# Optimization experiments

Hardware: AMD Instinct MI355X
Metric: run time of the kernel (lower is better)

## Reference

```python
import jax, jax.numpy as jnp
import numpy as np

N_POINTS = 1048576
FEATURES = 64
RES = 256


def setup_inputs() -> dict:
    key = jax.random.key(0)
    k1, k2, k3, k4 = jax.random.split(key, 4)
    x = jax.random.uniform(k1, (N_POINTS, 3), jnp.float32, -1.0, 1.0)
    plane_xy = jax.random.normal(k2, (1, FEATURES, RES, RES), jnp.float32)
    plane_xz = jax.random.normal(k3, (1, FEATURES, RES, RES), jnp.float32)
    plane_yz = jax.random.normal(k4, (1, FEATURES, RES, RES), jnp.float32)
    pose = jnp.zeros((1,), jnp.float32)
    person_id = 0
    return {"x": x, "plane_xy": plane_xy, "plane_xz": plane_xz,
            "plane_yz": plane_yz, "pose": pose, "person_id": person_id}


def _grid_sample_points(plane, uv):
    """Bilinear sample. plane: [1,C,IH,IW], uv: [N,2] in [-1,1]. Returns [N,C].
    Matches the hand-rolled torch grid_sample (align_corners=True semantics,
    corner indices clamped, weights computed from unclamped floor coords)."""
    C, IH, IW = plane.shape[1], plane.shape[2], plane.shape[3]
    ix = (uv[:, 0] + 1.0) * 0.5 * (IW - 1)
    iy = (uv[:, 1] + 1.0) * 0.5 * (IH - 1)
    fx0 = jnp.floor(ix)
    fy0 = jnp.floor(iy)
    # bilinear weights (differentiable w.r.t. ix, iy)
    w_nw = (fx0 + 1.0 - ix) * (fy0 + 1.0 - iy)
    w_ne = (ix - fx0) * (fy0 + 1.0 - iy)
    w_sw = (fx0 + 1.0 - ix) * (iy - fy0)
    w_se = (ix - fx0) * (iy - fy0)
    # clamped integer corner indices (non-differentiable, as in torch no_grad)
    x0 = jnp.clip(fx0, 0, IW - 1).astype(jnp.int32)
    x1 = jnp.clip(fx0 + 1.0, 0, IW - 1).astype(jnp.int32)
    y0 = jnp.clip(fy0, 0, IH - 1).astype(jnp.int32)
    y1 = jnp.clip(fy0 + 1.0, 0, IH - 1).astype(jnp.int32)
    pf = plane.reshape(C, IH * IW)  # [C, IH*IW]
    v_nw = pf[:, y0 * IW + x0]  # [C, N]
    v_ne = pf[:, y0 * IW + x1]
    v_sw = pf[:, y1 * IW + x0]
    v_se = pf[:, y1 * IW + x1]
    out = v_nw * w_nw + v_ne * w_ne + v_sw * w_sw + v_se * w_se  # [C, N]
    return out.T  # [N, C]


def reference(x, plane_xy, plane_xz, plane_yz, pose, person_id):
    # person_id selects the (single) person's planes; pose is unused upstream.
    feat_xy = _grid_sample_points(plane_xy, x[:, [0, 1]])
    feat_xz = _grid_sample_points(plane_xz, x[:, [0, 2]])
    feat_yz = _grid_sample_points(plane_yz, x[:, [1, 2]])
    feat = (feat_xy + feat_xz + feat_yz) / 3.0  # [N, FEATURES]
    return feat
```

## Files before the change

### kernel.cpp

```cpp
#include <hip/hip_runtime.h>

#define N_POINTS 1048576
#define FEAT 64
#define RES 256
#define PLANE_ELEMS (FEAT * RES * RES)

#define BUCKET_G 32
#define NBUCKET (BUCKET_G * BUCKET_G * BUCKET_G)

#define SAMPLE_BLOCKS (N_POINTS / 32)
#define SAMPLE_CPX (SAMPLE_BLOCKS / 8)

typedef unsigned short ushort_t;
typedef float v4f __attribute__((ext_vector_type(4)));

__device__ __forceinline__ ushort_t f2bf(float f) {
  unsigned u = __float_as_uint(f);
  unsigned r = u + 0x7FFFu + ((u >> 16) & 1u);
  return (ushort_t)(r >> 16);
}

__global__ __launch_bounds__(256) void transpose_bf16(
    const float* __restrict__ pxy, const float* __restrict__ pxz,
    const float* __restrict__ pyz, ushort_t* __restrict__ dst) {
  __shared__ ushort_t tile[64][72];
  const int plane = blockIdx.y;
  const float* src = (plane == 0) ? pxy : ((plane == 1) ? pxz : pyz);
  ushort_t* out = dst + (size_t)plane * PLANE_ELEMS;
  const int p0 = blockIdx.x * 64;
  const int tid = threadIdx.x;
#pragma unroll
  for (int k = 0; k < 4; ++k) {
    int c = (tid >> 4) + k * 16;
    int pp = (tid & 15) * 4;
    float4 v = *(const float4*)(src + (size_t)c * (RES * RES) + p0 + pp);
    tile[pp + 0][c] = f2bf(v.x);
    tile[pp + 1][c] = f2bf(v.y);
    tile[pp + 2][c] = f2bf(v.z);
    tile[pp + 3][c] = f2bf(v.w);
  }
  __syncthreads();
#pragma unroll
  for (int k = 0; k < 2; ++k) {
    int idx = k * 256 + tid;
    int pp = idx >> 3;
    int c8 = (idx & 7) * 8;
    uint4 v = *(const uint4*)&tile[pp][c8];
    *(uint4*)(out + (size_t)(p0 + pp) * FEAT + c8) = v;
  }
}

__device__ __forceinline__ unsigned part1by2(unsigned v) {
  v &= 0x3FFu;
  v = (v | (v << 16)) & 0x030000FFu;
  v = (v | (v << 8)) & 0x0300F00Fu;
  v = (v | (v << 4)) & 0x030C30C3u;
  v = (v | (v << 2)) & 0x09249249u;
  return v;
}

__device__ __forceinline__ unsigned morton_bucket(float px, float py, float pz) {
  int bx = (int)((px + 1.0f) * (0.5f * BUCKET_G));
  int by = (int)((py + 1.0f) * (0.5f * BUCKET_G));
  int bz = (int)((pz + 1.0f) * (0.5f * BUCKET_G));
  bx = min(max(bx, 0), BUCKET_G - 1);
  by = min(max(by, 0), BUCKET_G - 1);
  bz = min(max(bz, 0), BUCKET_G - 1);
  return part1by2((unsigned)bx) | (part1by2((unsigned)by) << 1) |
         (part1by2((unsigned)bz) << 2);
}

__global__ __launch_bounds__(256) void zero_hist(unsigned* __restrict__ h) {
  h[blockIdx.x * 256 + threadIdx.x] = 0u;
}

__global__ __launch_bounds__(256) void bucket_count(
    const float* __restrict__ x, unsigned* __restrict__ hist) {
  int n = blockIdx.x * 256 + threadIdx.x;
  float px = x[n * 3 + 0];
  float py = x[n * 3 + 1];
  float pz = x[n * 3 + 2];
  atomicAdd(&hist[morton_bucket(px, py, pz)], 1u);
}

__global__ __launch_bounds__(1024) void scan_hist(
    const unsigned* __restrict__ hist, unsigned* __restrict__ cursor) {
  __shared__ unsigned part[1024];
  const int tid = threadIdx.x;
  unsigned local[32];
  unsigned s = 0;
#pragma unroll
  for (int i = 0; i < 32; ++i) {
    local[i] = s;
    s += hist[tid * 32 + i];
  }
  part[tid] = s;
  __syncthreads();
  for (int off = 1; off < 1024; off <<= 1) {
    unsigned add = (tid >= off) ? part[tid - off] : 0u;
    __syncthreads();
    part[tid] += add;
    __syncthreads();
  }
  unsigned base = (tid == 0) ? 0u : part[tid - 1];
#pragma unroll
  for (int i = 0; i < 32; ++i) cursor[tid * 32 + i] = base + local[i];
}

__global__ __launch_bounds__(256) void bucket_scatter(
    const float* __restrict__ x, unsigned* __restrict__ cursor,
    float4* __restrict__ xs) {
  int n = blockIdx.x * 256 + threadIdx.x;
  float px = x[n * 3 + 0];
  float py = x[n * 3 + 1];
  float pz = x[n * 3 + 2];
  unsigned b = morton_bucket(px, py, pz);
  unsigned pos = atomicAdd(&cursor[b], 1u);
  xs[pos] = make_float4(px, py, pz, __uint_as_float((unsigned)n));
}

__device__ __forceinline__ void unpack_fma(uint4 v, float w, float* acc) {
  acc[0] = fmaf(__uint_as_float(v.x << 16), w, acc[0]);
  acc[1] = fmaf(__uint_as_float(v.x & 0xFFFF0000u), w, acc[1]);
  acc[2] = fmaf(__uint_as_float(v.y << 16), w, acc[2]);
  acc[3] = fmaf(__uint_as_float(v.y & 0xFFFF0000u), w, acc[3]);
  acc[4] = fmaf(__uint_as_float(v.z << 16), w, acc[4]);
  acc[5] = fmaf(__uint_as_float(v.z & 0xFFFF0000u), w, acc[5]);
  acc[6] = fmaf(__uint_as_float(v.w << 16), w, acc[6]);
  acc[7] = fmaf(__uint_as_float(v.w & 0xFFFF0000u), w, acc[7]);
}

__device__ __forceinline__ void sample_plane(const ushort_t* __restrict__ tp,
                                             float u, float v, int c8,
                                             float* acc) {
  float ix = (u + 1.0f) * 0.5f * (float)(RES - 1);
  float iy = (v + 1.0f) * 0.5f * (float)(RES - 1);
  float fx0 = floorf(ix), fy0 = floorf(iy);
  float wx1 = ix - fx0, wy1 = iy - fy0;
  float wx0 = fx0 + 1.0f - ix, wy0 = fy0 + 1.0f - iy;
  int x0 = min(max((int)fx0, 0), RES - 1);
  int y0 = min(max((int)fy0, 0), RES - 1);
  int x1 = min(max((int)fx0 + 1, 0), RES - 1);
  int y1 = min(max((int)fy0 + 1, 0), RES - 1);

  const uint4 v00 = *(const uint4*)(tp + (size_t)(y0 * RES + x0) * FEAT + c8);
  const uint4 v01 = *(const uint4*)(tp + (size_t)(y0 * RES + x1) * FEAT + c8);
  const uint4 v10 = *(const uint4*)(tp + (size_t)(y1 * RES + x0) * FEAT + c8);
  const uint4 v11 = *(const uint4*)(tp + (size_t)(y1 * RES + x1) * FEAT + c8);

  unpack_fma(v00, wx0 * wy0, acc);
  unpack_fma(v01, wx1 * wy0, acc);
  unpack_fma(v10, wx0 * wy1, acc);
  unpack_fma(v11, wx1 * wy1, acc);
}

__global__ __launch_bounds__(256) void triplane_sample_sorted(
    const float4* __restrict__ xs, const ushort_t* __restrict__ tps,
    float* __restrict__ out) {
  int bid = blockIdx.x;
  int swz = (bid & 7) * SAMPLE_CPX + (bid >> 3);
  int p = swz * 32 + (threadIdx.x >> 3);
  int c8 = (threadIdx.x & 7) << 3;

  v4f pt = __builtin_nontemporal_load((const v4f*)xs + p);
  unsigned n = __float_as_uint(pt.w);

  float acc[8] = {0.f, 0.f, 0.f, 0.f, 0.f, 0.f, 0.f, 0.f};
  sample_plane(tps, pt.x, pt.y, c8, acc);
  sample_plane(tps + PLANE_ELEMS, pt.x, pt.z, c8, acc);
  sample_plane(tps + 2 * PLANE_ELEMS, pt.y, pt.z, c8, acc);

  const float s = 1.0f / 3.0f;
  v4f lo = {acc[0] * s, acc[1] * s, acc[2] * s, acc[3] * s};
  v4f hi = {acc[4] * s, acc[5] * s, acc[6] * s, acc[7] * s};
  float* o = out + (size_t)n * FEAT + c8;
  __builtin_nontemporal_store(lo, (v4f*)o);
  __builtin_nontemporal_store(hi, (v4f*)(o + 4));
}

__global__ __launch_bounds__(256) void triplane_sample_bf16(
    const float* __restrict__ x, const ushort_t* __restrict__ tps,
    float* __restrict__ out) {
  int t = blockIdx.x * 256 + threadIdx.x;
  int n = t >> 3;
  int c8 = (t & 7) << 3;
  float px = __builtin_nontemporal_load(x + n * 3 + 0);
  float py = __builtin_nontemporal_load(x + n * 3 + 1);
  float pz = __builtin_nontemporal_load(x + n * 3 + 2);
  float acc[8] = {0.f, 0.f, 0.f, 0.f, 0.f, 0.f, 0.f, 0.f};
  sample_plane(tps, px, py, c8, acc);
  sample_plane(tps + PLANE_ELEMS, px, pz, c8, acc);
  sample_plane(tps + 2 * PLANE_ELEMS, py, pz, c8, acc);
  const float s = 1.0f / 3.0f;
  v4f lo = {acc[0] * s, acc[1] * s, acc[2] * s, acc[3] * s};
  v4f hi = {acc[4] * s, acc[5] * s, acc[6] * s, acc[7] * s};
  float* o = out + (size_t)n * FEAT + c8;
  __builtin_nontemporal_store(lo, (v4f*)o);
  __builtin_nontemporal_store(hi, (v4f*)(o + 4));
}

__device__ __forceinline__ float sample_one(const float* __restrict__ pc,
                                            float u, float v) {
  float ix = (u + 1.0f) * 0.5f * (float)(RES - 1);
  float iy = (v + 1.0f) * 0.5f * (float)(RES - 1);
  float fx0 = floorf(ix), fy0 = floorf(iy);
  float wx1 = ix - fx0, wy1 = iy - fy0;
  float wx0 = fx0 + 1.0f - ix, wy0 = fy0 + 1.0f - iy;
  int x0 = min(max((int)fx0, 0), RES - 1);
  int y0 = min(max((int)fy0, 0), RES - 1);
  int x1 = min(max((int)fx0 + 1, 0), RES - 1);
  int y1 = min(max((int)fy0 + 1, 0), RES - 1);
  return pc[y0 * RES + x0] * (wx0 * wy0) + pc[y0 * RES + x1] * (wx1 * wy0) +
         pc[y1 * RES + x0] * (wx0 * wy1) + pc[y1 * RES + x1] * (wx1 * wy1);
}

__global__ __launch_bounds__(256) void triplane_direct(
    const float* __restrict__ x, const float* __restrict__ pxy,
    const float* __restrict__ pxz, const float* __restrict__ pyz,
    float* __restrict__ out) {
  int t = blockIdx.x * 256 + threadIdx.x;
  int n = t >> 6;
  int c = t & 63;
  float px = x[n * 3 + 0];
  float py = x[n * 3 + 1];
  float pz = x[n * 3 + 2];
  const size_t cs = (size_t)c * (RES * RES);
  float acc = sample_one(pxy + cs, px, py) + sample_one(pxz + cs, px, pz) +
              sample_one(pyz + cs, py, pz);
  out[(size_t)n * FEAT + c] = acc * (1.0f / 3.0f);
}

extern "C" void kernel_launch(void* const* d_in, const int* in_sizes, int n_in,
                              void* d_out, int out_size, void* d_ws,
                              size_t ws_size, hipStream_t stream) {
  const float* x   = (const float*)d_in[0];
  const float* pxy = (const float*)d_in[1];
  const float* pxz = (const float*)d_in[2];
  const float* pyz = (const float*)d_in[3];
  float* out = (float*)d_out;

  const size_t tps_bytes = (size_t)3 * PLANE_ELEMS * sizeof(ushort_t);
  const size_t xs_bytes  = (size_t)N_POINTS * sizeof(float4);
  const size_t cnt_bytes = (size_t)NBUCKET * sizeof(unsigned);
  const size_t need_sorted = tps_bytes + xs_bytes + 2 * cnt_bytes;

  if (ws_size >= need_sorted) {
    ushort_t* tps    = (ushort_t*)d_ws;
    float4* xs       = (float4*)((char*)d_ws + tps_bytes);
    unsigned* cursor = (unsigned*)((char*)d_ws + tps_bytes + xs_bytes);
    unsigned* hist   = cursor + NBUCKET;

    dim3 tgrid(RES * RES / 64, 3);
    transpose_bf16<<<tgrid, 256, 0, stream>>>(pxy, pxz, pyz, tps);
    zero_hist<<<NBUCKET / 256, 256, 0, stream>>>(hist);
    bucket_count<<<N_POINTS / 256, 256, 0, stream>>>(x, hist);
    scan_hist<<<1, 1024, 0, stream>>>(hist, cursor);
    bucket_scatter<<<N_POINTS / 256, 256, 0, stream>>>(x, cursor, xs);
    triplane_sample_sorted<<<SAMPLE_BLOCKS, 256, 0, stream>>>(xs, tps, out);
  } else if (ws_size >= tps_bytes) {
    ushort_t* tps = (ushort_t*)d_ws;
    dim3 tgrid(RES * RES / 64, 3);
    transpose_bf16<<<tgrid, 256, 0, stream>>>(pxy, pxz, pyz, tps);
    triplane_sample_bf16<<<(N_POINTS * 8) / 256, 256, 0, stream>>>(x, tps, out);
  } else {
    triplane_direct<<<(N_POINTS * 64) / 256, 256, 0, stream>>>(x, pxy, pxz,
                                                               pyz, out);
  }
}
```

Before: 481.3 us.

## Fuse plane transpose with bucket count and store plane cache as fp16

```diff
diff --git a/kernel.cpp b/kernel.cpp
--- a/kernel.cpp
+++ b/kernel.cpp
@@ -11,43 +11,17 @@
 #define SAMPLE_BLOCKS (N_POINTS / 32)
 #define SAMPLE_CPX (SAMPLE_BLOCKS / 8)
 
+#define TRANSPOSE_BLOCKS (3 * (RES * RES / 64))
+#define COUNT_BLOCKS (N_POINTS / 256)
+#define PREP_BLOCKS (TRANSPOSE_BLOCKS + COUNT_BLOCKS)
+
 typedef unsigned short ushort_t;
 typedef float v4f __attribute__((ext_vector_type(4)));
-
-__device__ __forceinline__ ushort_t f2bf(float f) {
-  unsigned u = __float_as_uint(f);
-  unsigned r = u + 0x7FFFu + ((u >> 16) & 1u);
-  return (ushort_t)(r >> 16);
-}
-
-__global__ __launch_bounds__(256) void transpose_bf16(
-    const float* __restrict__ pxy, const float* __restrict__ pxz,
-    const float* __restrict__ pyz, ushort_t* __restrict__ dst) {
-  __shared__ ushort_t tile[64][72];
-  const int plane = blockIdx.y;
-  const float* src = (plane == 0) ? pxy : ((plane == 1) ? pxz : pyz);
-  ushort_t* out = dst + (size_t)plane * PLANE_ELEMS;
-  const int p0 = blockIdx.x * 64;
-  const int tid = threadIdx.x;
-#pragma unroll
-  for (int k = 0; k < 4; ++k) {
-    int c = (tid >> 4) + k * 16;
-    int pp = (tid & 15) * 4;
-    float4 v = *(const float4*)(src + (size_t)c * (RES * RES) + p0 + pp);
-    tile[pp + 0][c] = f2bf(v.x);
-    tile[pp + 1][c] = f2bf(v.y);
-    tile[pp + 2][c] = f2bf(v.z);
-    tile[pp + 3][c] = f2bf(v.w);
-  }
-  __syncthreads();
-#pragma unroll
-  for (int k = 0; k < 2; ++k) {
-    int idx = k * 256 + tid;
-    int pp = idx >> 3;
-    int c8 = (idx & 7) * 8;
-    uint4 v = *(const uint4*)&tile[pp][c8];
-    *(uint4*)(out + (size_t)(p0 + pp) * FEAT + c8) = v;
-  }
+typedef _Float16 half8 __attribute__((ext_vector_type(8)));
+
+__device__ __forceinline__ ushort_t f2h(float f) {
+  _Float16 h = (_Float16)f;
+  return __builtin_bit_cast(unsigned short, h);
 }
 
 __device__ __forceinline__ unsigned part1by2(unsigned v) {
@@ -70,17 +44,45 @@
          (part1by2((unsigned)bz) << 2);
 }
 
-__global__ __launch_bounds__(256) void zero_hist(unsigned* __restrict__ h) {
-  h[blockIdx.x * 256 + threadIdx.x] = 0u;
-}
-
-__global__ __launch_bounds__(256) void bucket_count(
+__global__ __launch_bounds__(256) void prep_transpose_count(
+    const float* __restrict__ pxy, const float* __restrict__ pxz,
+    const float* __restrict__ pyz, ushort_t* __restrict__ dst,
     const float* __restrict__ x, unsigned* __restrict__ hist) {
-  int n = blockIdx.x * 256 + threadIdx.x;
-  float px = x[n * 3 + 0];
-  float py = x[n * 3 + 1];
-  float pz = x[n * 3 + 2];
-  atomicAdd(&hist[morton_bucket(px, py, pz)], 1u);
+  const int b = blockIdx.x;
+  const int tid = threadIdx.x;
+  if (b >= TRANSPOSE_BLOCKS) {
+    int n = (b - TRANSPOSE_BLOCKS) * 256 + tid;
+    float px = x[n * 3 + 0];
+    float py = x[n * 3 + 1];
+    float pz = x[n * 3 + 2];
+    atomicAdd(&hist[morton_bucket(px, py, pz)], 1u);
+    return;
+  }
+  __shared__ ushort_t tile[64][72];
+  const int plane = b >> 10;
+  const int p0 = (b & 1023) * 64;
+  const float* src = (plane == 0) ? pxy : ((plane == 1) ? pxz : pyz);
+  ushort_t* out = dst + (size_t)plane * PLANE_ELEMS;
+#pragma unroll
+  for (int k = 0; k < 4; ++k) {
+    int c = (tid >> 4) + k * 16;
+    int pp = (tid & 15) * 4;
+    v4f v = __builtin_nontemporal_load(
+        (const v4f*)(src + (size_t)c * (RES * RES) + p0 + pp));
+    tile[pp + 0][c] = f2h(v.x);
+    tile[pp + 1][c] = f2h(v.y);
+    tile[pp + 2][c] = f2h(v.z);
+    tile[pp + 3][c] = f2h(v.w);
+  }
+  __syncthreads();
+#pragma unroll
+  for (int k = 0; k < 2; ++k) {
+    int idx = k * 256 + tid;
+    int pp = idx >> 3;
+    int c8 = (idx & 7) * 8;
+    uint4 v = *(const uint4*)&tile[pp][c8];
+    *(uint4*)(out + (size_t)(p0 + pp) * FEAT + c8) = v;
+  }
 }
 
 __global__ __launch_bounds__(1024) void scan_hist(
@@ -119,22 +121,16 @@
   xs[pos] = make_float4(px, py, pz, __uint_as_float((unsigned)n));
 }
 
-__device__ __forceinline__ void unpack_fma(uint4 v, float w, float* acc) {
-  acc[0] = fmaf(__uint_as_float(v.x << 16), w, acc[0]);
-  acc[1] = fmaf(__uint_as_float(v.x & 0xFFFF0000u), w, acc[1]);
-  acc[2] = fmaf(__uint_as_float(v.y << 16), w, acc[2]);
-  acc[3] = fmaf(__uint_as_float(v.y & 0xFFFF0000u), w, acc[3]);
-  acc[4] = fmaf(__uint_as_float(v.z << 16), w, acc[4]);
-  acc[5] = fmaf(__uint_as_float(v.z & 0xFFFF0000u), w, acc[5]);
-  acc[6] = fmaf(__uint_as_float(v.w << 16), w, acc[6]);
-  acc[7] = fmaf(__uint_as_float(v.w & 0xFFFF0000u), w, acc[7]);
+__device__ __forceinline__ void fma_mix8(half8 v, float w, float* acc) {
+#pragma unroll
+  for (int j = 0; j < 8; ++j) acc[j] = fmaf((float)v[j], w, acc[j]);
 }
 
 __device__ __forceinline__ void sample_plane(const ushort_t* __restrict__ tp,
                                              float u, float v, int c8,
                                              float* acc) {
-  float ix = (u + 1.0f) * 0.5f * (float)(RES - 1);
-  float iy = (v + 1.0f) * 0.5f * (float)(RES - 1);
+  float ix = fmaf(u, 0.5f * (float)(RES - 1), 0.5f * (float)(RES - 1));
+  float iy = fmaf(v, 0.5f * (float)(RES - 1), 0.5f * (float)(RES - 1));
   float fx0 = floorf(ix), fy0 = floorf(iy);
   float wx1 = ix - fx0, wy1 = iy - fy0;
   float wx0 = fx0 + 1.0f - ix, wy0 = fy0 + 1.0f - iy;
@@ -143,15 +139,15 @@
   int x1 = min(max((int)fx0 + 1, 0), RES - 1);
   int y1 = min(max((int)fy0 + 1, 0), RES - 1);
 
-  const uint4 v00 = *(const uint4*)(tp + (size_t)(y0 * RES + x0) * FEAT + c8);
-  const uint4 v01 = *(const uint4*)(tp + (size_t)(y0 * RES + x1) * FEAT + c8);
-  const uint4 v10 = *(const uint4*)(tp + (size_t)(y1 * RES + x0) * FEAT + c8);
-  const uint4 v11 = *(const uint4*)(tp + (size_t)(y1 * RES + x1) * FEAT + c8);
-
-  unpack_fma(v00, wx0 * wy0, acc);
-  unpack_fma(v01, wx1 * wy0, acc);
-  unpack_fma(v10, wx0 * wy1, acc);
-  unpack_fma(v11, wx1 * wy1, acc);
+  const half8 v00 = *(const half8*)(tp + (size_t)(y0 * RES + x0) * FEAT + c8);
+  const half8 v01 = *(const half8*)(tp + (size_t)(y0 * RES + x1) * FEAT + c8);
+  const half8 v10 = *(const half8*)(tp + (size_t)(y1 * RES + x0) * FEAT + c8);
+  const half8 v11 = *(const half8*)(tp + (size_t)(y1 * RES + x1) * FEAT + c8);
+
+  fma_mix8(v00, wx0 * wy0, acc);
+  fma_mix8(v01, wx1 * wy0, acc);
+  fma_mix8(v10, wx0 * wy1, acc);
+  fma_mix8(v11, wx1 * wy1, acc);
 }
 
 __global__ __launch_bounds__(256) void triplane_sample_sorted(
@@ -178,7 +174,37 @@
   __builtin_nontemporal_store(hi, (v4f*)(o + 4));
 }
 
-__global__ __launch_bounds__(256) void triplane_sample_bf16(
+__global__ __launch_bounds__(256) void transpose_only(
+    const float* __restrict__ pxy, const float* __restrict__ pxz,
+    const float* __restrict__ pyz, ushort_t* __restrict__ dst) {
+  __shared__ ushort_t tile[64][72];
+  const int plane = blockIdx.y;
+  const float* src = (plane == 0) ? pxy : ((plane == 1) ? pxz : pyz);
+  ushort_t* out = dst + (size_t)plane * PLANE_ELEMS;
+  const int p0 = blockIdx.x * 64;
+  const int tid = threadIdx.x;
+#pragma unroll
+  for (int k = 0; k < 4; ++k) {
+    int c = (tid >> 4) + k * 16;
+    int pp = (tid & 15) * 4;
+    v4f v = *(const v4f*)(src + (size_t)c * (RES * RES) + p0 + pp);
+    tile[pp + 0][c] = f2h(v.x);
+    tile[pp + 1][c] = f2h(v.y);
+    tile[pp + 2][c] = f2h(v.z);
+    tile[pp + 3][c] = f2h(v.w);
+  }
+  __syncthreads();
+#pragma unroll
+  for (int k = 0; k < 2; ++k) {
+    int idx = k * 256 + tid;
+    int pp = idx >> 3;
+    int c8 = (idx & 7) * 8;
+    uint4 v = *(const uint4*)&tile[pp][c8];
+    *(uint4*)(out + (size_t)(p0 + pp) * FEAT + c8) = v;
+  }
+}
+
+__global__ __launch_bounds__(256) void triplane_sample_f16(
     const float* __restrict__ x, const ushort_t* __restrict__ tps,
     float* __restrict__ out) {
   int t = blockIdx.x * 256 + threadIdx.x;
@@ -250,18 +276,17 @@
     unsigned* cursor = (unsigned*)((char*)d_ws + tps_bytes + xs_bytes);
     unsigned* hist   = cursor + NBUCKET;
 
-    dim3 tgrid(RES * RES / 64, 3);
-    transpose_bf16<<<tgrid, 256, 0, stream>>>(pxy, pxz, pyz, tps);
-    zero_hist<<<NBUCKET / 256, 256, 0, stream>>>(hist);
-    bucket_count<<<N_POINTS / 256, 256, 0, stream>>>(x, hist);
+    (void)hipMemsetAsync(hist, 0, cnt_bytes, stream);
+    prep_transpose_count<<<PREP_BLOCKS, 256, 0, stream>>>(pxy, pxz, pyz, tps,
+                                                          x, hist);
     scan_hist<<<1, 1024, 0, stream>>>(hist, cursor);
     bucket_scatter<<<N_POINTS / 256, 256, 0, stream>>>(x, cursor, xs);
     triplane_sample_sorted<<<SAMPLE_BLOCKS, 256, 0, stream>>>(xs, tps, out);
   } else if (ws_size >= tps_bytes) {
     ushort_t* tps = (ushort_t*)d_ws;
     dim3 tgrid(RES * RES / 64, 3);
-    transpose_bf16<<<tgrid, 256, 0, stream>>>(pxy, pxz, pyz, tps);
-    triplane_sample_bf16<<<(N_POINTS * 8) / 256, 256, 0, stream>>>(x, tps, out);
+    transpose_only<<<tgrid, 256, 0, stream>>>(pxy, pxz, pyz, tps);
+    triplane_sample_f16<<<(N_POINTS * 8) / 256, 256, 0, stream>>>(x, tps, out);
   } else {
     triplane_direct<<<(N_POINTS * 64) / 256, 256, 0, stream>>>(x, pxy, pxz,
                                                                pyz, out);
```

Result: no change. 472.5 us (-1.8%).
